# Optimization experiments

Measured on AMD Instinct MI355X. Metric: run time of the kernel, lower is better.

Reference implementation:

```python
import jax, jax.numpy as jnp
import numpy as np

NUM_COARSE = 1024

def sqdist(a, b):
    # a: [..., N, 3], b: [..., M, 3] -> [..., N, M] squared euclidean distances
    d = (jnp.sum(a * a, -1)[..., :, None] + jnp.sum(b * b, -1)[..., None, :]
         - 2.0 * jnp.einsum('...nd,...md->...nm', a, b))
    return jnp.maximum(d, 0.0)

def fps_idx(pts, n_samples):
    # pts: [N, 3]; farthest point sampling starting from index 0 (pn2 convention)
    d0 = jnp.sum((pts - pts[0]) ** 2, -1)  # [N]
    def step(dists, _):
        idx = jnp.argmax(dists)
        d = jnp.sum((pts - pts[idx]) ** 2, -1)
        return jnp.minimum(dists, d), idx
    _, idxs = jax.lax.scan(step, d0, None, length=n_samples - 1)
    return jnp.concatenate([jnp.zeros((1,), jnp.int32), idxs.astype(jnp.int32)])

def emd_dist(x, y, eps, iters):
    # x, y: [n, 3] equal-cardinality clouds. Approximate optimal assignment via
    # log-domain entropic OT (eps = regularization, iters = iterations), then
    # per-point squared distance to the matched point (as in the auction EMD kernel).
    n = x.shape[0]
    C = sqdist(x, y)                       # [n, n]
    Cs = jax.lax.stop_gradient(C)          # assignment is a constant wrt grads
    loga = -jnp.log(jnp.float32(n))
    def step(f, _):
        g = -eps * jax.nn.logsumexp((f[:, None] - Cs) / eps + loga, axis=0)
        f = -eps * jax.nn.logsumexp((g[None, :] - Cs) / eps + loga, axis=1)
        return f, None
    f, _ = jax.lax.scan(step, jnp.zeros((n,), Cs.dtype), None, length=iters)
    g = -eps * jax.nn.logsumexp((f[:, None] - Cs) / eps + loga, axis=0)
    assign = jnp.argmax(f[:, None] + g[None, :] - Cs, axis=1)  # [n]
    return jnp.take_along_axis(C, assign[:, None], axis=1)[:, 0]

def chamfer(a, b):
    # a: [B, N, 3], b: [B, M, 3] -> per-point min squared dists ([B,N], [B,M])
    C = sqdist(a, b)
    return jnp.min(C, axis=2), jnp.min(C, axis=1)

def setup_inputs() -> dict:
    key = jax.random.key(0)
    k1, k2, k3 = jax.random.split(key, 3)
    return {
        'output1': jax.random.uniform(k1, (4, NUM_COARSE, 3), jnp.float32),
        'output2': jax.random.uniform(k2, (4, 4096, 3), jnp.float32),
        'gt': jax.random.uniform(k3, (4, 4096, 3), jnp.float32),
        'eps': jnp.float32(0.005),
        'iters': 10,
    }

def reference(output1, output2, gt, eps, iters):
    gt = gt[:, :, :3]
    # --- EMD branch ---
    idx = jax.vmap(lambda p: fps_idx(p, NUM_COARSE))(gt)            # [B, num_coarse]
    gt_fps = jnp.take_along_axis(gt, idx[:, :, None], axis=1)       # [B, num_coarse, 3]
    d1 = jax.vmap(lambda x, y: emd_dist(x, y, eps, iters))(output1, gt_fps)
    emd1 = jnp.sqrt(d1).mean(1)
    d2 = jax.vmap(lambda x, y: emd_dist(x, y, eps, iters))(output2, gt)
    emd2 = jnp.sqrt(d2).mean(1)
    # --- Chamfer branch ---
    d11, d12 = chamfer(gt, output1)
    cd_p1 = (jnp.sqrt(d11).mean(1) + jnp.sqrt(d12).mean(1)) / 2
    cd_t1 = d11.mean(1) + d12.mean(1)
    d21, d22 = chamfer(gt, output2)
    cd_p2 = (jnp.sqrt(d21).mean(1) + jnp.sqrt(d22).mean(1)) / 2
    cd_t2 = d21.mean(1) + d22.mean(1)
    return (output1, output2, emd1, emd2, cd_p1, cd_p2, cd_t1, cd_t2)
```

## Files before the change

kernel.cpp:

```cpp
#include <hip/hip_runtime.h>
#include <math.h>


#define LOG2E 1.4426950408889634f
#define LN2   0.6931471805599453f
#define NEGBIG -3.0e38f

#define SY2(b) ((b) * 512)
#define SYF(b) (2048 + (b) * 16)
#define SYD(b) (2112 + (b) * 16)

#if __has_builtin(__builtin_amdgcn_exp2f)
__device__ __forceinline__ float fexp2(float x) { return __builtin_amdgcn_exp2f(x); }
#else
__device__ __forceinline__ float fexp2(float x) { return exp2f(x); }
#endif

__device__ __forceinline__ float dist_rn(float x, float y, float z,
                                         float qx, float qy, float qz) {
  float dx = __fsub_rn(x, qx), dy = __fsub_rn(y, qy), dz = __fsub_rn(z, qz);
  return __fadd_rn(__fadd_rn(__fmul_rn(dx, dx), __fmul_rn(dy, dy)),
                   __fmul_rn(dz, dz));
}

struct FpsS {
  float4 sq[4096];
  unsigned long long xch[4][2];
  float4 sOut[64];
};
struct WorkS {
  float4 ldsRow[256];
  float4 ldsC[1024];
  float ldsG2[1024];
  float red[8];
};
struct Emd1S {
  float4 rowsO[1024];
  float4 rowsG[1024];
  float2 part[16][64];
  float g2[1024];
  float red[8];
};
union SmemAll {
  FpsS f;
  WorkS w;
  Emd1S e;
  float pad_force_one_block_per_cu[21504];
};

struct UniArgs {
  const float* gt;
  const float* epsP;
  const float4 *o1P4, *o2P4, *gtP4;
  float4* gfP4;
  float2 *gpart2, *fpart2, *apart2;
  unsigned long long* vecT;
  unsigned* sync;
  float* out;
  int NC2, BPB;
};

__device__ __forceinline__ void bar_signal(unsigned* slot, unsigned val) {
  __syncthreads();
  if (threadIdx.x == 0)
    __hip_atomic_store(slot, val, __ATOMIC_RELEASE, __HIP_MEMORY_SCOPE_AGENT);
}
template <int SLP>
__device__ __forceinline__ void bar_waitall(const unsigned* base, int n,
                                            unsigned target) {
  if (threadIdx.x < 64) {
    int l = threadIdx.x;
    for (;;) {
      unsigned v = (l < n)
                       ? __hip_atomic_load(base + l * 16, __ATOMIC_RELAXED,
                                           __HIP_MEMORY_SCOPE_AGENT)
                       : target;
      if (__all((int)(v >= target))) break;
      __builtin_amdgcn_s_sleep(SLP);
    }
    if (l == 0)
      (void)__hip_atomic_load(base, __ATOMIC_ACQUIRE, __HIP_MEMORY_SCOPE_AGENT);
  }
  __syncthreads();
}

__device__ __forceinline__ float blockRedSum(float v, float* red4) {
#pragma unroll
  for (int m = 32; m; m >>= 1) v += __shfl_xor(v, m, 64);
  int lane = threadIdx.x & 63, wid = threadIdx.x >> 6;
  __syncthreads();
  if (lane == 0) red4[wid] = v;
  __syncthreads();
  float s = 0.0f;
  if (threadIdx.x == 0) {
#pragma unroll
    for (int w = 0; w < 4; ++w) s += red4[w];
  }
  return s;
}

__device__ __forceinline__ void poll4(const unsigned long long* v, int tid,
                                      unsigned want, float* w0, float* w1,
                                      float* w2, float* w3) {
  unsigned long long p0, p1, p2, p3;
  for (;;) {
    p0 = __hip_atomic_load(v + tid, __ATOMIC_RELAXED, __HIP_MEMORY_SCOPE_AGENT);
    p1 = __hip_atomic_load(v + tid + 256, __ATOMIC_RELAXED, __HIP_MEMORY_SCOPE_AGENT);
    p2 = __hip_atomic_load(v + tid + 512, __ATOMIC_RELAXED, __HIP_MEMORY_SCOPE_AGENT);
    p3 = __hip_atomic_load(v + tid + 768, __ATOMIC_RELAXED, __HIP_MEMORY_SCOPE_AGENT);
    if ((unsigned)(p0 >> 32) >= want && (unsigned)(p1 >> 32) >= want &&
        (unsigned)(p2 >> 32) >= want && (unsigned)(p3 >> 32) >= want)
      break;
    __builtin_amdgcn_s_sleep(1);
  }
  *w0 = __uint_as_float((unsigned)p0);
  *w1 = __uint_as_float((unsigned)p1);
  *w2 = __uint_as_float((unsigned)p2);
  *w3 = __uint_as_float((unsigned)p3);
}

__device__ void warm_spin(const UniArgs& A) {
  float a0 = (float)(threadIdx.x + 1), a1 = a0 + 0.5f, a2 = a0 + 1.5f,
        a3 = a0 + 2.5f;
  const unsigned* sy = A.sync;
  for (;;) {
    unsigned d0 = __hip_atomic_load(sy + SYD(0), __ATOMIC_RELAXED, __HIP_MEMORY_SCOPE_AGENT);
    unsigned d1 = __hip_atomic_load(sy + SYD(1), __ATOMIC_RELAXED, __HIP_MEMORY_SCOPE_AGENT);
    unsigned d2 = __hip_atomic_load(sy + SYD(2), __ATOMIC_RELAXED, __HIP_MEMORY_SCOPE_AGENT);
    unsigned d3 = __hip_atomic_load(sy + SYD(3), __ATOMIC_RELAXED, __HIP_MEMORY_SCOPE_AGENT);
    if ((d0 & d1 & d2 & d3) != 0u) break;
#pragma unroll
    for (int i = 0; i < 64; ++i) {
      a0 = fmaf(a0, 1.0000001f, 1.0e-6f);
      a1 = fmaf(a1, 1.0000001f, 1.0e-6f);
      a2 = fmaf(a2, 1.0000001f, 1.0e-6f);
      a3 = fmaf(a3, 1.0000001f, 1.0e-6f);
    }
  }
  asm volatile("" ::"v"(a0), "v"(a1), "v"(a2), "v"(a3));
}

__global__ __launch_bounds__(256) void prep_kernel(
    const float* __restrict__ o1, const float* __restrict__ o2,
    const float* __restrict__ gt, const float* __restrict__ epsP,
    float4* __restrict__ o1P4, float4* __restrict__ o2P4,
    float4* __restrict__ gtP4) {
  int id = blockIdx.x * 256 + threadIdx.x;
  float eps = *epsP;
  float se = (1.0f / eps) * LOG2E;
  float kxy = sqrtf(se + se);
  const float* src;
  float4* dst;
  if (id < 4096) { src = o1 + 3 * id; dst = o1P4 + id; }
  else if (id < 20480) { int p = id - 4096; src = o2 + 3 * p; dst = o2P4 + p; }
  else { int p = id - 20480; src = gt + 3 * p; dst = gtP4 + p; }
  float x = src[0], y = src[1], z = src[2];
  float xx = x * x + y * y + z * z;
  *dst = make_float4(kxy * x, kxy * y, kxy * z, xx * se);
}

template <int NC>
__device__ __forceinline__ float finalize_w(const float2* __restrict__ part,
                                            int gi, int stride, float nloga2) {
  float2 pp[NC];
#pragma unroll
  for (int c = 0; c < NC; ++c) pp[c] = part[c * stride + gi];
  float m = pp[0].x;
#pragma unroll
  for (int c = 1; c < NC; ++c) m = fmaxf(m, pp[c].x);
  float s = 0.0f;
#pragma unroll
  for (int c = 0; c < NC; ++c) s += pp[c].y * fexp2(pp[c].x - m);
  return nloga2 - (m + __log2f(s));
}

template <int NC>
__device__ void pass2_job(int b, int cb, int ch, const float4* __restrict__ rowP,
                          const float4* __restrict__ colP,
                          const float2* __restrict__ vpart,
                          float2* __restrict__ dst, float4* ldsRow) {
  const int CH = 4096 / NC;
  int tid = threadIdx.x;
  int gj = b * 4096 + cb * 2048 + tid;
  float cx[8], cy[8], cz[8];
#pragma unroll
  for (int c = 0; c < 8; ++c) {
    float4 cp = colP[gj + (c << 8)];
    cx[c] = cp.x; cy[c] = cp.y; cz[c] = cp.z;
  }
  float M[8], S[8];
#pragma unroll
  for (int c = 0; c < 8; ++c) { M[c] = NEGBIG; S[c] = 0.0f; }
  int r0 = ch * CH;
  for (int t0 = 0; t0 < CH; t0 += 256) {
    __syncthreads();
    {
      int gi = b * 4096 + r0 + t0 + tid;
      float4 rp = rowP[gi];
      float w = vpart ? finalize_w<NC>(vpart, gi, 16384, 12.0f) : -rp.w;
      ldsRow[tid] = make_float4(rp.x, rp.y, rp.z, w);
    }
    __syncthreads();
#pragma unroll 1
    for (int r = 0; r < 256; r += 8) {
      float4 q[8];
#pragma unroll
      for (int u = 0; u < 8; ++u) q[u] = ldsRow[r + u];
#pragma unroll
      for (int c = 0; c < 8; ++c) {
        float t[8];
#pragma unroll
        for (int u = 0; u < 8; ++u)
          t[u] = fmaf(cx[c], q[u].x, fmaf(cy[c], q[u].y, fmaf(cz[c], q[u].z, q[u].w)));
        float cm = fmaxf(fmaxf(fmaxf(t[0], t[1]), fmaxf(t[2], t[3])),
                         fmaxf(fmaxf(t[4], t[5]), fmaxf(t[6], t[7])));
        float nM = fmaxf(M[c], cm);
        float s8 = ((fexp2(t[0] - nM) + fexp2(t[1] - nM)) +
                    (fexp2(t[2] - nM) + fexp2(t[3] - nM))) +
                   ((fexp2(t[4] - nM) + fexp2(t[5] - nM)) +
                    (fexp2(t[6] - nM) + fexp2(t[7] - nM)));
        S[c] = fmaf(S[c], fexp2(M[c] - nM), s8);
        M[c] = nM;
      }
    }
  }
#pragma unroll
  for (int c = 0; c < 8; ++c)
    dst[ch * 16384 + gj + (c << 8)] = make_float2(M[c], S[c]);
}

__device__ void cham_job(const float4* __restrict__ aP, const float4* __restrict__ bP,
                         int Na, int Nb, float* outP, float* outT,
                         float scaleP, float scaleT, int b, int rb,
                         WorkS& w, const float* epsP) {
  int tid = threadIdx.x;
  int i0 = rb * 512 + tid, i1 = i0 + 256;
  float4 a0 = aP[b * Na + i0], a1 = aP[b * Na + i1];
  float m0 = 3.0e38f, m1 = 3.0e38f;
  for (int t0 = 0; t0 < Nb; t0 += 1024) {
    __syncthreads();
    for (int t = tid; t < 1024; t += 256) w.ldsC[t] = bP[b * Nb + t0 + t];
    __syncthreads();
#pragma unroll 4
    for (int t = 0; t < 1024; ++t) {
      float4 q = w.ldsC[t];
      float c0 = fmaf(-a0.z, q.z, fmaf(-a0.y, q.y, fmaf(-a0.x, q.x, q.w + a0.w)));
      float c1 = fmaf(-a1.z, q.z, fmaf(-a1.y, q.y, fmaf(-a1.x, q.x, q.w + a1.w)));
      m0 = fminf(m0, c0);
      m1 = fminf(m1, c1);
    }
  }
  float eps = *epsP;
  float inv_se = eps * LN2;
  float d0 = fmaxf(0.0f, m0 * inv_se), d1 = fmaxf(0.0f, m1 * inv_se);
  float s1 = blockRedSum(sqrtf(d0) + sqrtf(d1), w.red);
  float s2 = blockRedSum(d0 + d1, w.red);
  if (tid == 0) {
    atomicAdd(outP, s1 * scaleP);
    atomicAdd(outT, s2 * scaleT);
  }
}

__device__ void chamfer_worker(int g, const UniArgs& A, WorkS& w) {
  for (int cj = g; cj < 104; cj += 88) {
    if (cj < 32) {
      cham_job(A.gtP4, A.o2P4, 4096, 4096, A.out + 61452 + (cj >> 3),
               A.out + 61460 + (cj >> 3), 1.0f / 8192.0f, 1.0f / 4096.0f,
               cj >> 3, cj & 7, w, A.epsP);
    } else if (cj < 64) {
      int j = cj - 32;
      cham_job(A.o2P4, A.gtP4, 4096, 4096, A.out + 61452 + (j >> 3),
               A.out + 61460 + (j >> 3), 1.0f / 8192.0f, 1.0f / 4096.0f,
               j >> 3, j & 7, w, A.epsP);
    } else if (cj < 96) {
      int j = cj - 64;
      cham_job(A.gtP4, A.o1P4, 4096, 1024, A.out + 61448 + (j >> 3),
               A.out + 61456 + (j >> 3), 1.0f / 8192.0f, 1.0f / 4096.0f,
               j >> 3, j & 7, w, A.epsP);
    } else {
      int j = cj - 96;
      cham_job(A.o1P4, A.gtP4, 1024, 4096, A.out + 61448 + (j >> 1),
               A.out + 61456 + (j >> 1), 1.0f / 2048.0f, 1.0f / 1024.0f,
               j >> 1, j & 1, w, A.epsP);
    }
  }
}

template <int NC>
__device__ void assign2_job(int b, int cc, int rb, const UniArgs& A, WorkS& w) {
  int tid = threadIdx.x;
  __syncthreads();
  for (int t = tid; t < 1024; t += 256) {
    int gjc = b * 4096 + cc * 1024 + t;
    float wv = finalize_w<NC>(A.gpart2, gjc, 16384, 12.0f);
    float4 qp = A.gtP4[gjc];
    w.ldsC[t] = make_float4(qp.x, qp.y, qp.z, wv);
    w.ldsG2[t] = wv + qp.w;
  }
  __syncthreads();
#pragma unroll
  for (int rr = 0; rr < 2; ++rr) {
    int gi = b * 4096 + rb * 512 + (rr << 8) + tid;
    float4 rp = A.o2P4[gi];
    float rx = rp.x, ry = rp.y, rz = rp.z, xw = rp.w;
    float bW = NEGBIG;
    int bj = 0;
    for (int t = 0; t < 1024; ++t) {
      float4 q = w.ldsC[t];
      float W = fmaf(rz, q.z, fmaf(ry, q.y, fmaf(rx, q.x, q.w - xw)));
      W = fminf(W, w.ldsG2[t]);
      if (W > bW) { bW = W; bj = cc * 1024 + t; }
    }
    A.apart2[cc * 16384 + gi] = make_float2(bW, __int_as_float(bj));
  }
}

__device__ void combine2_job(int b, int rb, const UniArgs& A, WorkS& w) {
  int tid = threadIdx.x;
  int gi = b * 4096 + (rb << 8) + tid;
  float bW = NEGBIG;
  int bj = 0;
#pragma unroll
  for (int c = 0; c < 4; ++c) {
    float2 p = A.apart2[c * 16384 + gi];
    if (p.x > bW) { bW = p.x; bj = __float_as_int(p.y); }
  }
  float eps = *A.epsP;
  float inv_se = eps * LN2;
  float4 rp = A.o2P4[gi];
  float4 qp = A.gtP4[b * 4096 + bj];
  float dotp = rp.x * qp.x + rp.y * qp.y + rp.z * qp.z;
  float d = fmaxf(0.0f, (rp.w + qp.w - dotp) * inv_se);
  float s = blockRedSum(sqrtf(d), w.red);
  if (tid == 0) atomicAdd(A.out + 61444 + b, s * (1.0f / 4096.0f));
}

__device__ void fps_role(const UniArgs& A, int b, FpsS& f) {
  int tid = threadIdx.x;
  const float* base = A.gt + b * 12288;
  for (int t = tid; t < 4096; t += 256) {
    float x = base[3 * t], y = base[3 * t + 1], z = base[3 * t + 2];
    f.sq[t] = make_float4(x, y, z, x * x + y * y + z * z);
  }
  if (tid < 8) ((unsigned long long*)f.xch)[tid] = 0ull;
  __syncthreads();
  float eps = *A.epsP;
  float se = (1.0f / eps) * LOG2E;
  float kxy = sqrtf(se + se);
  float4 p0 = f.sq[0];
  float px[16], py[16], pz[16], d[16];
#pragma unroll
  for (int k = 0; k < 16; ++k) {
    float4 p = f.sq[tid + (k << 8)];
    px[k] = p.x; py[k] = p.y; pz[k] = p.z;
    d[k] = dist_rn(p.x, p.y, p.z, p0.x, p0.y, p0.z);
  }
  if (tid == 0)
    f.sOut[0] = make_float4(kxy * p0.x, kxy * p0.y, kxy * p0.z, p0.w * se);
  int lane = tid & 63, w = tid >> 6;
  float qx = p0.x, qy = p0.y, qz = p0.z;
  unsigned long long* xmine = &f.xch[w][0];

#define DPPSTEP(C)                                                             \
  {                                                                            \
    unsigned ov = (unsigned)__builtin_amdgcn_update_dpp(0, (int)bvu, C, 0xf,  \
                                                        0xf, true);           \
    int oi = __builtin_amdgcn_update_dpp(0, bi, C, 0xf, 0xf, true);           \
    bool t = (ov > bvu) || ((ov == bvu) && ((unsigned)oi < (unsigned)bi));    \
    bvu = t ? ov : bvu;                                                        \
    bi = t ? oi : bi;                                                          \
  }
#define SCOMB(VV, II)                                                          \
  {                                                                            \
    unsigned _v = (unsigned)(VV);                                              \
    int _i = (II);                                                             \
    if (_v > wv || (_v == wv && _i < wi)) { wv = _v; wi = _i; }                \
  }
#define XCOMB(G)                                                               \
  {                                                                            \
    unsigned _v = (unsigned)((G) >> 32);                                       \
    int _i = (int)((unsigned)(G) & 0xFFFu);                                    \
    if (_v > bv2 || (_v == bv2 && _i < bi2)) { bv2 = _v; bi2 = _i; }          \
  }

#pragma unroll 1
  for (int s = 1; s < 1024; ++s) {
    if ((s & 63) == 0 && tid < 64)
      A.gfP4[(b << 10) + (s - 64) + tid] = f.sOut[tid];
    float tv[8]; int ti[8];
#pragma unroll
    for (int i = 0; i < 8; ++i) {
      int k0 = 2 * i, k1 = 2 * i + 1;
      float n0 = fminf(d[k0], dist_rn(px[k0], py[k0], pz[k0], qx, qy, qz));
      float n1 = fminf(d[k1], dist_rn(px[k1], py[k1], pz[k1], qx, qy, qz));
      d[k0] = n0; d[k1] = n1;
      bool t = n1 > n0;
      tv[i] = t ? n1 : n0;
      ti[i] = tid + ((t ? k1 : k0) << 8);
    }
    float uv[4]; int ui[4];
#pragma unroll
    for (int i = 0; i < 4; ++i) {
      bool t = tv[2 * i + 1] > tv[2 * i];
      uv[i] = t ? tv[2 * i + 1] : tv[2 * i];
      ui[i] = t ? ti[2 * i + 1] : ti[2 * i];
    }
    bool tA = uv[1] > uv[0];
    float vA = tA ? uv[1] : uv[0]; int iA = tA ? ui[1] : ui[0];
    bool tB = uv[3] > uv[2];
    float vB = tB ? uv[3] : uv[2]; int iB = tB ? ui[3] : ui[2];
    bool tC = vB > vA;
    float bv = tC ? vB : vA; int bi = tC ? iB : iA;
    unsigned bvu = __float_as_uint(bv);
    DPPSTEP(0xB1)
    DPPSTEP(0x4E)
    DPPSTEP(0x141)
    DPPSTEP(0x140)
    unsigned wv = (unsigned)__builtin_amdgcn_readlane((int)bvu, 0);
    int wi = __builtin_amdgcn_readlane(bi, 0);
    SCOMB(__builtin_amdgcn_readlane((int)bvu, 16), __builtin_amdgcn_readlane(bi, 16))
    SCOMB(__builtin_amdgcn_readlane((int)bvu, 32), __builtin_amdgcn_readlane(bi, 32))
    SCOMB(__builtin_amdgcn_readlane((int)bvu, 48), __builtin_amdgcn_readlane(bi, 48))
    int par = s & 1;
    unsigned tagw = (unsigned)(s & 1023);
    unsigned long long mine = ((unsigned long long)wv << 32) |
                              ((unsigned long long)tagw << 16) |
                              (unsigned long long)(unsigned)wi;
    if (lane == 0)
      __hip_atomic_store(xmine + par, mine, __ATOMIC_RELAXED,
                         __HIP_MEMORY_SCOPE_WORKGROUP);
    unsigned long long g1, g2, g3;
    for (;;) {
      g1 = __hip_atomic_load(&f.xch[(w + 1) & 3][par], __ATOMIC_RELAXED,
                             __HIP_MEMORY_SCOPE_WORKGROUP);
      g2 = __hip_atomic_load(&f.xch[(w + 2) & 3][par], __ATOMIC_RELAXED,
                             __HIP_MEMORY_SCOPE_WORKGROUP);
      g3 = __hip_atomic_load(&f.xch[(w + 3) & 3][par], __ATOMIC_RELAXED,
                             __HIP_MEMORY_SCOPE_WORKGROUP);
      if ((((unsigned)(g1 >> 16) & 1023u) == tagw) &
          (((unsigned)(g2 >> 16) & 1023u) == tagw) &
          (((unsigned)(g3 >> 16) & 1023u) == tagw))
        break;
    }
    unsigned bv2 = wv; int bi2 = wi;
    XCOMB(g1) XCOMB(g2) XCOMB(g3)
    float4 q = f.sq[bi2];
    qx = q.x; qy = q.y; qz = q.z;
    if (tid == 0)
      f.sOut[s & 63] = make_float4(kxy * qx, kxy * qy, kxy * qz, q.w * se);
  }
#undef DPPSTEP
#undef SCOMB
#undef XCOMB
  if (tid < 64) A.gfP4[(b << 10) + 960 + tid] = f.sOut[tid];
  bar_signal(A.sync + SYF(b), 1u);
}

__device__ void emd1_role(int eb, int chunk, const UniArgs& A, Emd1S& m) {
  int tid = threadIdx.x;
  bar_waitall<16>(A.sync + SYF(eb), 1, 1u);
  for (int t = tid; t < 1024; t += 256) {
    float4 p = A.o1P4[eb * 1024 + t];
    m.rowsO[t] = make_float4(p.x, p.y, p.z, -p.w);
    m.rowsG[t] = A.gfP4[eb * 1024 + t];
  }
  int lane = tid & 63, rl = tid >> 6;
  int col = chunk * 64 + lane;
  float4 cG = A.gfP4[eb * 1024 + col];
  float4 cO = A.o1P4[eb * 1024 + col];
  unsigned long long* gv = A.vecT + (eb << 10);
  unsigned long long* fv = A.vecT + 4096 + (eb << 10);

  for (int s = 1; s <= 21; ++s) {
    int odd = s & 1;
    if (s >= 2) {
      const unsigned long long* v = odd ? fv : gv;
      float4* rows = odd ? m.rowsO : m.rowsG;
      float w0, w1, w2, w3;
      poll4(v, tid, (unsigned)(s - 1), &w0, &w1, &w2, &w3);
      rows[tid].w = w0;
      rows[tid + 256].w = w1;
      rows[tid + 512].w = w2;
      rows[tid + 768].w = w3;
    }
    __syncthreads();
    const float4* rows = odd ? m.rowsO : m.rowsG;
    float cx = odd ? cG.x : cO.x;
    float cy = odd ? cG.y : cO.y;
    float cz = odd ? cG.z : cO.z;
#pragma unroll 1
    for (int k = 0; k < 4; ++k) {
      int ch = rl * 4 + k;
      float M = NEGBIG, S = 0.0f;
      int r0 = ch * 64;
#pragma unroll 1
      for (int r = 0; r < 64; r += 8) {
        float4 q[8];
#pragma unroll
        for (int u = 0; u < 8; ++u) q[u] = rows[r0 + r + u];
        float t8[8];
#pragma unroll
        for (int u = 0; u < 8; ++u)
          t8[u] = fmaf(cx, q[u].x, fmaf(cy, q[u].y, fmaf(cz, q[u].z, q[u].w)));
        float cm = fmaxf(fmaxf(fmaxf(t8[0], t8[1]), fmaxf(t8[2], t8[3])),
                         fmaxf(fmaxf(t8[4], t8[5]), fmaxf(t8[6], t8[7])));
        float nM = fmaxf(M, cm);
        float s8 = ((fexp2(t8[0] - nM) + fexp2(t8[1] - nM)) +
                    (fexp2(t8[2] - nM) + fexp2(t8[3] - nM))) +
                   ((fexp2(t8[4] - nM) + fexp2(t8[5] - nM)) +
                    (fexp2(t8[6] - nM) + fexp2(t8[7] - nM)));
        S = fmaf(S, fexp2(M - nM), s8);
        M = nM;
      }
      m.part[ch][lane] = make_float2(M, S);
    }
    __syncthreads();
    if (tid < 64) {
      float2 pp[16];
#pragma unroll
      for (int c = 0; c < 16; ++c) pp[c] = m.part[c][tid];
      float mm = pp[0].x;
#pragma unroll
      for (int c = 1; c < 16; ++c) mm = fmaxf(mm, pp[c].x);
      float ss = 0.0f;
#pragma unroll
      for (int c = 0; c < 16; ++c) ss += pp[c].y * fexp2(pp[c].x - mm);
      float w = 10.0f - (mm + __log2f(ss));
      unsigned long long pk = ((unsigned long long)(unsigned)s << 32) |
                              (unsigned long long)__float_as_uint(w);
      __hip_atomic_store((odd ? gv : fv) + col, pk, __ATOMIC_RELAXED,
                         __HIP_MEMORY_SCOPE_AGENT);
    }
  }
  __syncthreads();

  {
    float w0, w1, w2, w3;
    poll4(gv, tid, 21u, &w0, &w1, &w2, &w3);
    float4 qp0 = A.gfP4[eb * 1024 + tid];
    float4 qp1 = A.gfP4[eb * 1024 + tid + 256];
    float4 qp2 = A.gfP4[eb * 1024 + tid + 512];
    float4 qp3 = A.gfP4[eb * 1024 + tid + 768];
    m.rowsG[tid] = make_float4(qp0.x, qp0.y, qp0.z, w0);
    m.g2[tid] = w0 + qp0.w;
    m.rowsG[tid + 256] = make_float4(qp1.x, qp1.y, qp1.z, w1);
    m.g2[tid + 256] = w1 + qp1.w;
    m.rowsG[tid + 512] = make_float4(qp2.x, qp2.y, qp2.z, w2);
    m.g2[tid + 512] = w2 + qp2.w;
    m.rowsG[tid + 768] = make_float4(qp3.x, qp3.y, qp3.z, w3);
    m.g2[tid + 768] = w3 + qp3.w;
  }
  __syncthreads();
  float eps = *A.epsP;
  float inv_se = eps * LN2;
  int rw = tid & 63, qc = tid >> 6;
  int gi = eb * 1024 + chunk * 64 + rw;
  float4 rp = A.o1P4[gi];
  float rx = rp.x, ry = rp.y, rz = rp.z, xw = rp.w;
  float bW = NEGBIG;
  int bj = 0;
  int t0 = qc * 256;
  for (int t = t0; t < t0 + 256; ++t) {
    float4 q = m.rowsG[t];
    float W = fmaf(rz, q.z, fmaf(ry, q.y, fmaf(rx, q.x, q.w - xw)));
    W = fminf(W, m.g2[t]);
    if (W > bW) { bW = W; bj = t; }
  }
  m.part[qc][rw] = make_float2(bW, __int_as_float(bj));
  __syncthreads();
  if (tid < 64) {
    float2 p0 = m.part[0][tid];
    float vb = p0.x;
    int vj = __float_as_int(p0.y);
#pragma unroll
    for (int c = 1; c < 4; ++c) {
      float2 p = m.part[c][tid];
      if (p.x > vb) { vb = p.x; vj = __float_as_int(p.y); }
    }
    float4 qp = A.gfP4[eb * 1024 + vj];
    float dotp = rp.x * qp.x + rp.y * qp.y + rp.z * qp.z;
    float dd = fmaxf(0.0f, (rp.w + qp.w - dotp) * inv_se);
    float v = sqrtf(dd);
#pragma unroll
    for (int mk = 32; mk; mk >>= 1) v += __shfl_xor(v, mk, 64);
    if (tid == 0) atomicAdd(A.out + 61440 + eb, v * (1.0f / 1024.0f));
  }
  if (chunk == 0) bar_signal(A.sync + SYD(eb), 1u);
}

__global__ __launch_bounds__(256, 1) void uni_kernel(UniArgs A) {
  __shared__ SmemAll sm;
  int bid = blockIdx.x;
  if (bid < 4) {
    fps_role(A, bid, sm.f);
    return;
  }
  int e = bid - 4;
  int W = 4 * A.BPB;
  if (e < W) {
    int b = e / A.BPB, rest = e % A.BPB;
    int cb = rest / A.NC2, ch = rest % A.NC2;
    unsigned* slots = A.sync + SY2(b);
    for (int s = 1; s <= 21; ++s) {
      const float4 *rowP, *colP;
      const float2* vp;
      float2* dst;
      if (s & 1) { rowP = A.o2P4; colP = A.gtP4; vp = (s == 1) ? nullptr : A.fpart2; dst = A.gpart2; }
      else       { rowP = A.gtP4; colP = A.o2P4; vp = A.gpart2; dst = A.fpart2; }
      if (A.NC2 == 16) pass2_job<16>(b, cb, ch, rowP, colP, vp, dst, sm.w.ldsRow);
      else             pass2_job<8>(b, cb, ch, rowP, colP, vp, dst, sm.w.ldsRow);
      bar_signal(slots + rest * 16, (unsigned)s);
      bar_waitall<16>(slots, A.BPB, (unsigned)s);
    }
    for (int j = rest; j < 32; j += A.BPB) {
      int cc = j >> 3, rb = j & 7;
      if (A.NC2 == 16) assign2_job<16>(b, cc, rb, A, sm.w);
      else             assign2_job<8>(b, cc, rb, A, sm.w);
    }
    bar_signal(slots + rest * 16, 22u);
    bar_waitall<4>(slots, A.BPB, 22u);
    if (rest < 16) combine2_job(b, rest, A, sm.w);
    warm_spin(A);
    return;
  }
  int g = e - W;
  chamfer_worker(g, A, sm.w);
  if (g < 64) {
    emd1_role(g >> 4, g & 15, A, sm.e);
  } else {
    warm_spin(A);
  }
}

extern "C" void kernel_launch(void* const* d_in, const int* in_sizes, int n_in,
                              void* d_out, int out_size, void* d_ws, size_t ws_size,
                              hipStream_t stream) {
  (void)in_sizes; (void)n_in; (void)out_size;
  const float* o1 = (const float*)d_in[0];
  const float* o2 = (const float*)d_in[1];
  const float* gt = (const float*)d_in[2];
  const float* epsP = (const float*)d_in[3];
  float* out = (float*)d_out;
  float* ws = (float*)d_ws;

  int NC2 = 16;
  {
    size_t need16 = (size_t)(4096 + 16384 + 16384 + 65536 + 65536 + 16384 +
                             2 * (16 * 32768)) * 4;
    if (ws_size < need16) NC2 = 8;
  }
  size_t off = 0;
  unsigned* syncp = (unsigned*)(ws + off); off += 4096;
  unsigned long long* vecT = (unsigned long long*)(ws + off); off += 16384;
  float4* o1P4 = (float4*)(ws + off); off += 16384;
  float4* o2P4 = (float4*)(ws + off); off += 65536;
  float4* gtP4 = (float4*)(ws + off); off += 65536;
  float4* gfP4 = (float4*)(ws + off); off += 16384;
  float2* gpart2 = (float2*)(ws + off); off += (size_t)NC2 * 32768;
  float2* fpart2 = (float2*)(ws + off); off += (size_t)NC2 * 32768;
  float2* apart2 = fpart2;

  (void)hipMemcpyAsync(out, o1, 12288 * sizeof(float), hipMemcpyDeviceToDevice, stream);
  (void)hipMemcpyAsync(out + 12288, o2, 49152 * sizeof(float), hipMemcpyDeviceToDevice, stream);
  (void)hipMemsetAsync(out + 61440, 0, 24 * sizeof(float), stream);
  (void)hipMemsetAsync(syncp, 0, (4096 + 16384) * sizeof(float), stream);

  prep_kernel<<<144, 256, 0, stream>>>(o1, o2, gt, epsP, o1P4, o2P4, gtP4);

  UniArgs A;
  A.gt = gt; A.epsP = epsP;
  A.o1P4 = o1P4; A.o2P4 = o2P4; A.gtP4 = gtP4; A.gfP4 = gfP4;
  A.gpart2 = gpart2; A.fpart2 = fpart2; A.apart2 = apart2;
  A.vecT = vecT;
  A.sync = syncp; A.out = out;
  A.NC2 = NC2; A.BPB = 2 * NC2;
  int grid = 4 + 4 * A.BPB + 88;
  uni_kernel<<<grid, 256, 0, stream>>>(A);
}
```

Before: 1.163 ms.

## Pack FPS distance math into v_pk f32 ops and spin-wait with FMA bursts

The farthest-point-sampling inner loop now computes two candidate distances at once using packed v_pk_add_f32/v_pk_mul_f32 inline assembly on float2 vectors, halving VALU instruction count on the serial critical path. The EMD1 waiters switch from a sleeping barrier wait to a single-slot spin that runs FMA bursts, and the warm_spin burst length grows from 64 to 256 iterations. The FMA spinning appears meant to keep clocks high while the waiters idle, at the cost of power and of contending with the FPS block for issue slots. Packed adds of a negated query should match the rounded subtract, so results stay bit-identical.

```diff
diff --git a/kernel.cpp b/kernel.cpp
--- a/kernel.cpp
+++ b/kernel.cpp
@@ -9,6 +9,8 @@
 #define SY2(b) ((b) * 512)
 #define SYF(b) (2048 + (b) * 16)
 #define SYD(b) (2112 + (b) * 16)
+
+typedef float f32x2 __attribute__((ext_vector_type(2)));
 
 #if __has_builtin(__builtin_amdgcn_exp2f)
 __device__ __forceinline__ float fexp2(float x) { return __builtin_amdgcn_exp2f(x); }
@@ -119,9 +121,18 @@
   *w3 = __uint_as_float((unsigned)p3);
 }
 
+__device__ __forceinline__ void fma_burst(float* a) {
+#pragma unroll
+  for (int i = 0; i < 256; ++i) {
+    a[0] = fmaf(a[0], 1.0000001f, 1.0e-6f);
+    a[1] = fmaf(a[1], 1.0000001f, 1.0e-6f);
+    a[2] = fmaf(a[2], 1.0000001f, 1.0e-6f);
+    a[3] = fmaf(a[3], 1.0000001f, 1.0e-6f);
+  }
+}
+
 __device__ void warm_spin(const UniArgs& A) {
-  float a0 = (float)(threadIdx.x + 1), a1 = a0 + 0.5f, a2 = a0 + 1.5f,
-        a3 = a0 + 2.5f;
+  float a[4] = {(float)(threadIdx.x + 1), 1.5f, 2.5f, 3.5f};
   const unsigned* sy = A.sync;
   for (;;) {
     unsigned d0 = __hip_atomic_load(sy + SYD(0), __ATOMIC_RELAXED, __HIP_MEMORY_SCOPE_AGENT);
@@ -129,15 +140,22 @@
     unsigned d2 = __hip_atomic_load(sy + SYD(2), __ATOMIC_RELAXED, __HIP_MEMORY_SCOPE_AGENT);
     unsigned d3 = __hip_atomic_load(sy + SYD(3), __ATOMIC_RELAXED, __HIP_MEMORY_SCOPE_AGENT);
     if ((d0 & d1 & d2 & d3) != 0u) break;
-#pragma unroll
-    for (int i = 0; i < 64; ++i) {
-      a0 = fmaf(a0, 1.0000001f, 1.0e-6f);
-      a1 = fmaf(a1, 1.0000001f, 1.0e-6f);
-      a2 = fmaf(a2, 1.0000001f, 1.0e-6f);
-      a3 = fmaf(a3, 1.0000001f, 1.0e-6f);
-    }
-  }
-  asm volatile("" ::"v"(a0), "v"(a1), "v"(a2), "v"(a3));
+    fma_burst(a);
+  }
+  asm volatile("" ::"v"(a[0]), "v"(a[1]), "v"(a[2]), "v"(a[3]));
+}
+
+__device__ void warm_wait1(const unsigned* slot, unsigned target) {
+  float a[4] = {(float)(threadIdx.x + 1), 1.5f, 2.5f, 3.5f};
+  for (;;) {
+    unsigned v = __hip_atomic_load(slot, __ATOMIC_RELAXED, __HIP_MEMORY_SCOPE_AGENT);
+    if (v >= target) break;
+    fma_burst(a);
+  }
+  asm volatile("" ::"v"(a[0]), "v"(a[1]), "v"(a[2]), "v"(a[3]));
+  if (threadIdx.x == 0)
+    (void)__hip_atomic_load(slot, __ATOMIC_ACQUIRE, __HIP_MEMORY_SCOPE_AGENT);
+  __syncthreads();
 }
 
 __global__ __launch_bounds__(256) void prep_kernel(
@@ -348,11 +366,14 @@
   float se = (1.0f / eps) * LOG2E;
   float kxy = sqrtf(se + se);
   float4 p0 = f.sq[0];
-  float px[16], py[16], pz[16], d[16];
+  f32x2 PX[8], PY[8], PZ[8];
+  float d[16];
 #pragma unroll
   for (int k = 0; k < 16; ++k) {
     float4 p = f.sq[tid + (k << 8)];
-    px[k] = p.x; py[k] = p.y; pz[k] = p.z;
+    PX[k >> 1][k & 1] = p.x;
+    PY[k >> 1][k & 1] = p.y;
+    PZ[k >> 1][k & 1] = p.z;
     d[k] = dist_rn(p.x, p.y, p.z, p0.x, p0.y, p0.z);
   }
   if (tid == 0)
@@ -387,16 +408,29 @@
   for (int s = 1; s < 1024; ++s) {
     if ((s & 63) == 0 && tid < 64)
       A.gfP4[(b << 10) + (s - 64) + tid] = f.sOut[tid];
+    f32x2 qnx, qny, qnz;
+    qnx[0] = qnx[1] = -qx;
+    qny[0] = qny[1] = -qy;
+    qnz[0] = qnz[1] = -qz;
     float tv[8]; int ti[8];
 #pragma unroll
     for (int i = 0; i < 8; ++i) {
-      int k0 = 2 * i, k1 = 2 * i + 1;
-      float n0 = fminf(d[k0], dist_rn(px[k0], py[k0], pz[k0], qx, qy, qz));
-      float n1 = fminf(d[k1], dist_rn(px[k1], py[k1], pz[k1], qx, qy, qz));
-      d[k0] = n0; d[k1] = n1;
+      f32x2 dx, dy, dz, xx, yy, zz, ss, nn;
+      asm("v_pk_add_f32 %0, %1, %2" : "=v"(dx) : "v"(PX[i]), "v"(qnx));
+      asm("v_pk_add_f32 %0, %1, %2" : "=v"(dy) : "v"(PY[i]), "v"(qny));
+      asm("v_pk_add_f32 %0, %1, %2" : "=v"(dz) : "v"(PZ[i]), "v"(qnz));
+      asm("v_pk_mul_f32 %0, %1, %1" : "=v"(xx) : "v"(dx));
+      asm("v_pk_mul_f32 %0, %1, %1" : "=v"(yy) : "v"(dy));
+      asm("v_pk_mul_f32 %0, %1, %1" : "=v"(zz) : "v"(dz));
+      asm("v_pk_add_f32 %0, %1, %2" : "=v"(ss) : "v"(xx), "v"(yy));
+      asm("v_pk_add_f32 %0, %1, %2" : "=v"(nn) : "v"(ss), "v"(zz));
+      float n0 = fminf(d[2 * i], nn[0]);
+      float n1 = fminf(d[2 * i + 1], nn[1]);
+      d[2 * i] = n0;
+      d[2 * i + 1] = n1;
       bool t = n1 > n0;
       tv[i] = t ? n1 : n0;
-      ti[i] = tid + ((t ? k1 : k0) << 8);
+      ti[i] = tid + ((t ? (2 * i + 1) : (2 * i)) << 8);
     }
     float uv[4]; int ui[4];
 #pragma unroll
@@ -458,7 +492,7 @@
 
 __device__ void emd1_role(int eb, int chunk, const UniArgs& A, Emd1S& m) {
   int tid = threadIdx.x;
-  bar_waitall<16>(A.sync + SYF(eb), 1, 1u);
+  warm_wait1(A.sync + SYF(eb), 1u);
   for (int t = tid; t < 1024; t += 256) {
     float4 p = A.o1P4[eb * 1024 + t];
     m.rowsO[t] = make_float4(p.x, p.y, p.z, -p.w);
```

New measurement: 1.161 ms. About the same (-0.2%).

## Drop per-iteration block barrier in EMD sinkhorn loop and speculate FPS winner load

Applied to the files above, without the earlier changes.

The EMD role now has each wave poll only the 256 rows it will read and write their updated potentials itself, removing the block-wide __syncthreads at the top of each Sinkhorn half-step. The partial-result buffer is double-buffered by parity so the next step's writes cannot clobber the reduction still reading the previous one. In FPS, the cross-wave readlane combine becomes a balanced tree, and the wave's own winner coordinates are loaded speculatively before the inter-wave exchange. The initial FPS wait switches to a spin with FMA warm-up plus an acquire load. Correctness now depends on each wave reading only the rows it polled, which adds race risk.

```diff
diff --git a/kernel.cpp b/kernel.cpp
--- a/kernel.cpp
+++ b/kernel.cpp
@@ -37,7 +37,7 @@
 struct Emd1S {
   float4 rowsO[1024];
   float4 rowsG[1024];
-  float2 part[16][64];
+  float2 part[2][16][64];
   float g2[1024];
   float red[8];
 };
@@ -119,9 +119,18 @@
   *w3 = __uint_as_float((unsigned)p3);
 }
 
+__device__ __forceinline__ void fma_burst(float* a) {
+#pragma unroll
+  for (int i = 0; i < 64; ++i) {
+    a[0] = fmaf(a[0], 1.0000001f, 1.0e-6f);
+    a[1] = fmaf(a[1], 1.0000001f, 1.0e-6f);
+    a[2] = fmaf(a[2], 1.0000001f, 1.0e-6f);
+    a[3] = fmaf(a[3], 1.0000001f, 1.0e-6f);
+  }
+}
+
 __device__ void warm_spin(const UniArgs& A) {
-  float a0 = (float)(threadIdx.x + 1), a1 = a0 + 0.5f, a2 = a0 + 1.5f,
-        a3 = a0 + 2.5f;
+  float a[4] = {(float)(threadIdx.x + 1), 1.5f, 2.5f, 3.5f};
   const unsigned* sy = A.sync;
   for (;;) {
     unsigned d0 = __hip_atomic_load(sy + SYD(0), __ATOMIC_RELAXED, __HIP_MEMORY_SCOPE_AGENT);
@@ -129,15 +138,22 @@
     unsigned d2 = __hip_atomic_load(sy + SYD(2), __ATOMIC_RELAXED, __HIP_MEMORY_SCOPE_AGENT);
     unsigned d3 = __hip_atomic_load(sy + SYD(3), __ATOMIC_RELAXED, __HIP_MEMORY_SCOPE_AGENT);
     if ((d0 & d1 & d2 & d3) != 0u) break;
-#pragma unroll
-    for (int i = 0; i < 64; ++i) {
-      a0 = fmaf(a0, 1.0000001f, 1.0e-6f);
-      a1 = fmaf(a1, 1.0000001f, 1.0e-6f);
-      a2 = fmaf(a2, 1.0000001f, 1.0e-6f);
-      a3 = fmaf(a3, 1.0000001f, 1.0e-6f);
-    }
-  }
-  asm volatile("" ::"v"(a0), "v"(a1), "v"(a2), "v"(a3));
+    fma_burst(a);
+  }
+  asm volatile("" ::"v"(a[0]), "v"(a[1]), "v"(a[2]), "v"(a[3]));
+}
+
+__device__ void warm_wait1(const unsigned* slot, unsigned target) {
+  float a[4] = {(float)(threadIdx.x + 1), 1.5f, 2.5f, 3.5f};
+  for (;;) {
+    unsigned v = __hip_atomic_load(slot, __ATOMIC_RELAXED, __HIP_MEMORY_SCOPE_AGENT);
+    if (v >= target) break;
+    fma_burst(a);
+  }
+  asm volatile("" ::"v"(a[0]), "v"(a[1]), "v"(a[2]), "v"(a[3]));
+  if (threadIdx.x == 0)
+    (void)__hip_atomic_load(slot, __ATOMIC_ACQUIRE, __HIP_MEMORY_SCOPE_AGENT);
+  __syncthreads();
 }
 
 __global__ __launch_bounds__(256) void prep_kernel(
@@ -370,12 +386,6 @@
     bvu = t ? ov : bvu;                                                        \
     bi = t ? oi : bi;                                                          \
   }
-#define SCOMB(VV, II)                                                          \
-  {                                                                            \
-    unsigned _v = (unsigned)(VV);                                              \
-    int _i = (II);                                                             \
-    if (_v > wv || (_v == wv && _i < wi)) { wv = _v; wi = _i; }                \
-  }
 #define XCOMB(G)                                                               \
   {                                                                            \
     unsigned _v = (unsigned)((G) >> 32);                                       \
@@ -416,11 +426,20 @@
     DPPSTEP(0x4E)
     DPPSTEP(0x141)
     DPPSTEP(0x140)
-    unsigned wv = (unsigned)__builtin_amdgcn_readlane((int)bvu, 0);
-    int wi = __builtin_amdgcn_readlane(bi, 0);
-    SCOMB(__builtin_amdgcn_readlane((int)bvu, 16), __builtin_amdgcn_readlane(bi, 16))
-    SCOMB(__builtin_amdgcn_readlane((int)bvu, 32), __builtin_amdgcn_readlane(bi, 32))
-    SCOMB(__builtin_amdgcn_readlane((int)bvu, 48), __builtin_amdgcn_readlane(bi, 48))
+    unsigned r0v = (unsigned)__builtin_amdgcn_readlane((int)bvu, 0);
+    int r0i = __builtin_amdgcn_readlane(bi, 0);
+    unsigned r1v = (unsigned)__builtin_amdgcn_readlane((int)bvu, 16);
+    int r1i = __builtin_amdgcn_readlane(bi, 16);
+    unsigned r2v = (unsigned)__builtin_amdgcn_readlane((int)bvu, 32);
+    int r2i = __builtin_amdgcn_readlane(bi, 32);
+    unsigned r3v = (unsigned)__builtin_amdgcn_readlane((int)bvu, 48);
+    int r3i = __builtin_amdgcn_readlane(bi, 48);
+    bool tP = (r1v > r0v) || (r1v == r0v && r1i < r0i);
+    unsigned pv = tP ? r1v : r0v; int pi = tP ? r1i : r0i;
+    bool tQ = (r3v > r2v) || (r3v == r2v && r3i < r2i);
+    unsigned qv = tQ ? r3v : r2v; int qi = tQ ? r3i : r2i;
+    bool tR = (qv > pv) || (qv == pv && qi < pi);
+    unsigned wv = tR ? qv : pv; int wi = tR ? qi : pi;
     int par = s & 1;
     unsigned tagw = (unsigned)(s & 1023);
     unsigned long long mine = ((unsigned long long)wv << 32) |
@@ -429,6 +448,7 @@
     if (lane == 0)
       __hip_atomic_store(xmine + par, mine, __ATOMIC_RELAXED,
                          __HIP_MEMORY_SCOPE_WORKGROUP);
+    float4 mq = f.sq[wi];
     unsigned long long g1, g2, g3;
     for (;;) {
       g1 = __hip_atomic_load(&f.xch[(w + 1) & 3][par], __ATOMIC_RELAXED,
@@ -444,13 +464,14 @@
     }
     unsigned bv2 = wv; int bi2 = wi;
     XCOMB(g1) XCOMB(g2) XCOMB(g3)
-    float4 q = f.sq[bi2];
+    float4 q;
+    if (bv2 == wv && bi2 == wi) q = mq;
+    else q = f.sq[bi2];
     qx = q.x; qy = q.y; qz = q.z;
     if (tid == 0)
       f.sOut[s & 63] = make_float4(kxy * qx, kxy * qy, kxy * qz, q.w * se);
   }
 #undef DPPSTEP
-#undef SCOMB
 #undef XCOMB
   if (tid < 64) A.gfP4[(b << 10) + 960 + tid] = f.sOut[tid];
   bar_signal(A.sync + SYF(b), 1u);
@@ -458,7 +479,7 @@
 
 __device__ void emd1_role(int eb, int chunk, const UniArgs& A, Emd1S& m) {
   int tid = threadIdx.x;
-  bar_waitall<16>(A.sync + SYF(eb), 1, 1u);
+  warm_wait1(A.sync + SYF(eb), 1u);
   for (int t = tid; t < 1024; t += 256) {
     float4 p = A.o1P4[eb * 1024 + t];
     m.rowsO[t] = make_float4(p.x, p.y, p.z, -p.w);
@@ -470,20 +491,31 @@
   float4 cO = A.o1P4[eb * 1024 + col];
   unsigned long long* gv = A.vecT + (eb << 10);
   unsigned long long* fv = A.vecT + 4096 + (eb << 10);
+  __syncthreads();
 
   for (int s = 1; s <= 21; ++s) {
-    int odd = s & 1;
+    int odd = s & 1, par = s & 1;
     if (s >= 2) {
       const unsigned long long* v = odd ? fv : gv;
       float4* rows = odd ? m.rowsO : m.rowsG;
-      float w0, w1, w2, w3;
-      poll4(v, tid, (unsigned)(s - 1), &w0, &w1, &w2, &w3);
-      rows[tid].w = w0;
-      rows[tid + 256].w = w1;
-      rows[tid + 512].w = w2;
-      rows[tid + 768].w = w3;
-    }
-    __syncthreads();
+      unsigned want = (unsigned)(s - 1);
+      int rbase = rl * 256 + lane;
+      unsigned long long p0, p1, p2, p3;
+      for (;;) {
+        p0 = __hip_atomic_load(v + rbase, __ATOMIC_RELAXED, __HIP_MEMORY_SCOPE_AGENT);
+        p1 = __hip_atomic_load(v + rbase + 64, __ATOMIC_RELAXED, __HIP_MEMORY_SCOPE_AGENT);
+        p2 = __hip_atomic_load(v + rbase + 128, __ATOMIC_RELAXED, __HIP_MEMORY_SCOPE_AGENT);
+        p3 = __hip_atomic_load(v + rbase + 192, __ATOMIC_RELAXED, __HIP_MEMORY_SCOPE_AGENT);
+        if ((unsigned)(p0 >> 32) >= want && (unsigned)(p1 >> 32) >= want &&
+            (unsigned)(p2 >> 32) >= want && (unsigned)(p3 >> 32) >= want)
+          break;
+        __builtin_amdgcn_s_sleep(1);
+      }
+      rows[rbase].w = __uint_as_float((unsigned)p0);
+      rows[rbase + 64].w = __uint_as_float((unsigned)p1);
+      rows[rbase + 128].w = __uint_as_float((unsigned)p2);
+      rows[rbase + 192].w = __uint_as_float((unsigned)p3);
+    }
     const float4* rows = odd ? m.rowsO : m.rowsG;
     float cx = odd ? cG.x : cO.x;
     float cy = odd ? cG.y : cO.y;
@@ -495,13 +527,13 @@
       int r0 = ch * 64;
 #pragma unroll 1
       for (int r = 0; r < 64; r += 8) {
-        float4 q[8];
-#pragma unroll
-        for (int u = 0; u < 8; ++u) q[u] = rows[r0 + r + u];
+        float4 qq[8];
+#pragma unroll
+        for (int u = 0; u < 8; ++u) qq[u] = rows[r0 + r + u];
         float t8[8];
 #pragma unroll
         for (int u = 0; u < 8; ++u)
-          t8[u] = fmaf(cx, q[u].x, fmaf(cy, q[u].y, fmaf(cz, q[u].z, q[u].w)));
+          t8[u] = fmaf(cx, qq[u].x, fmaf(cy, qq[u].y, fmaf(cz, qq[u].z, qq[u].w)));
         float cm = fmaxf(fmaxf(fmaxf(t8[0], t8[1]), fmaxf(t8[2], t8[3])),
                          fmaxf(fmaxf(t8[4], t8[5]), fmaxf(t8[6], t8[7])));
         float nM = fmaxf(M, cm);
@@ -512,22 +544,22 @@
         S = fmaf(S, fexp2(M - nM), s8);
         M = nM;
       }
-      m.part[ch][lane] = make_float2(M, S);
+      m.part[par][ch][lane] = make_float2(M, S);
     }
     __syncthreads();
     if (tid < 64) {
       float2 pp[16];
 #pragma unroll
-      for (int c = 0; c < 16; ++c) pp[c] = m.part[c][tid];
+      for (int c = 0; c < 16; ++c) pp[c] = m.part[par][c][tid];
       float mm = pp[0].x;
 #pragma unroll
       for (int c = 1; c < 16; ++c) mm = fmaxf(mm, pp[c].x);
       float ss = 0.0f;
 #pragma unroll
       for (int c = 0; c < 16; ++c) ss += pp[c].y * fexp2(pp[c].x - mm);
-      float w = 10.0f - (mm + __log2f(ss));
+      float wq = 10.0f - (mm + __log2f(ss));
       unsigned long long pk = ((unsigned long long)(unsigned)s << 32) |
-                              (unsigned long long)__float_as_uint(w);
+                              (unsigned long long)__float_as_uint(wq);
       __hip_atomic_store((odd ? gv : fv) + col, pk, __ATOMIC_RELAXED,
                          __HIP_MEMORY_SCOPE_AGENT);
     }
@@ -566,15 +598,15 @@
     W = fminf(W, m.g2[t]);
     if (W > bW) { bW = W; bj = t; }
   }
-  m.part[qc][rw] = make_float2(bW, __int_as_float(bj));
+  m.part[0][qc][rw] = make_float2(bW, __int_as_float(bj));
   __syncthreads();
   if (tid < 64) {
-    float2 p0 = m.part[0][tid];
+    float2 p0 = m.part[0][0][tid];
     float vb = p0.x;
     int vj = __float_as_int(p0.y);
 #pragma unroll
     for (int c = 1; c < 4; ++c) {
-      float2 p = m.part[c][tid];
+      float2 p = m.part[0][c][tid];
       if (p.x > vb) { vb = p.x; vj = __float_as_int(p.y); }
     }
     float4 qp = A.gfP4[eb * 1024 + vj];
```

Measured after the change: 1.100 ms. 5.4% less time.
